# Performance work log

Measured on AMD Instinct MI355X. Metric: run time of the kernel, lower is better.

Reference implementation:

```python
import jax, jax.numpy as jnp
import numpy as np

B, N, D, U, S = 32, 1024, 2, 64, 2


def setup_inputs() -> dict:
    key = jax.random.key(0)
    ks = jax.random.split(key, 8)
    scale = 1.0 / np.sqrt(N)  # keep diffusion outputs in a sane range
    inputs = jax.random.normal(ks[0], (B, N, D), jnp.float32)
    supports = jax.random.normal(ks[1], (B, N, N, S), jnp.float32) * scale
    h_prev = jax.random.normal(ks[2], (B, N * U), jnp.float32)
    rows = (D + U) * (S + 1)  # 198
    wscale = 1.0 / np.sqrt(rows)
    r_kernel = jax.random.normal(ks[3], (rows, U), jnp.float32) * wscale
    u_kernel = jax.random.normal(ks[4], (rows, U), jnp.float32) * wscale
    c_kernel = jax.random.normal(ks[5], (rows, U), jnp.float32) * wscale
    zeros = jnp.zeros((U,), jnp.float32)
    return {"inputs": inputs, "supports": supports, "h_prev": h_prev,
            "r_kernel": r_kernel, "r_bias": zeros,
            "u_kernel": u_kernel, "u_bias": zeros,
            "c_kernel": c_kernel, "c_bias": zeros}


def _diff_conv(x_in, supports, state, kernel, bias):
    # x_in: (B,N,D), state: (B, N*U) -> output (B, N*U)
    b, n, _ = x_in.shape
    u = kernel.shape[1]
    x0 = jnp.concatenate([x_in, state.reshape(b, n, u)], axis=-1)  # (B,N,F)
    # batched graph diffusion for all S supports at once: (B,N,N,S)x(B,N,F)->(B,N,F,S)
    xm = jnp.einsum('bijs,bjf->bifs', supports, x0)
    x = jnp.concatenate([x0[..., None], xm], axis=-1)  # (B,N,F,M) matches tf stack+transpose order
    x = x.reshape(b * n, -1) @ kernel + bias  # (B*N, U)
    return x.reshape(b, n * u)


def reference(inputs, supports, h_prev, r_kernel, r_bias, u_kernel, u_bias, c_kernel, c_bias):
    r = jax.nn.sigmoid(_diff_conv(inputs, supports, h_prev, r_kernel, r_bias))
    u = jax.nn.sigmoid(_diff_conv(inputs, supports, h_prev, u_kernel, u_bias))
    c = jnp.tanh(_diff_conv(inputs, supports, r * h_prev, c_kernel, c_bias))
    h = u * h_prev + (1.0 - u) * c
    return h
```

## Files before the change

### kernel.cpp

```cpp
#include <hip/hip_runtime.h>
#include <hip/hip_bf16.h>

namespace {

constexpr int kN  = 1024;
constexpr int kU  = 64;
constexpr int kFP = 80;

typedef __attribute__((ext_vector_type(4))) float f32x4;
typedef __attribute__((ext_vector_type(8))) short sv8;
typedef unsigned int u32;
typedef unsigned short u16;

__device__ __forceinline__ u32 pack_bf2(float a, float b) {
  __hip_bfloat16 ha = __float2bfloat16(a);
  __hip_bfloat16 hb = __float2bfloat16(b);
  u16 ua = *reinterpret_cast<u16*>(&ha);
  u16 ub = *reinterpret_cast<u16*>(&hb);
  return (u32)ua | ((u32)ub << 16);
}

__device__ __forceinline__ u16 bf16bits(float a) {
  __hip_bfloat16 h = __float2bfloat16(a);
  return *reinterpret_cast<u16*>(&h);
}

__device__ __forceinline__ float bflo(u32 v) {
  u32 x = v << 16;
  return *reinterpret_cast<float*>(&x);
}
__device__ __forceinline__ float bfhi(u32 v) {
  u32 x = v & 0xffff0000u;
  return *reinterpret_cast<float*>(&x);
}

__device__ __forceinline__ void gl16(const void* g, void* l) {
  __builtin_amdgcn_global_load_lds(
      (const __attribute__((address_space(1))) u32*)g,
      (__attribute__((address_space(3))) u32*)l, 16, 0, 0);
}

__global__ __launch_bounds__(256) void convert_sup(
    const f32x4* __restrict__ sup4, uint2* __restrict__ outb) {
  const size_t n4 = (size_t)16 * 1024 * 1024;
  size_t idx = (size_t)blockIdx.x * 256 + threadIdx.x;
  const size_t stride = (size_t)gridDim.x * 256;
#pragma unroll 1
  for (; idx < n4; idx += stride) {
    f32x4 v = __builtin_nontemporal_load(sup4 + idx);
    uint2 o;
    o.x = pack_bf2(v[0], v[1]);
    o.y = pack_bf2(v[2], v[3]);
    outb[idx] = o;
  }
}

__global__ __launch_bounds__(256) void build_x0t(
    const float* __restrict__ inputs, const float* __restrict__ h_prev,
    __hip_bfloat16* __restrict__ x0t, __hip_bfloat16* __restrict__ x0tc) {
  const int bx = blockIdx.x;
  const int b  = bx >> 4;
  const int n0 = (bx & 15) * 64;
  const int t  = threadIdx.x;

  __shared__ float hp[64][65];

  const float* hpg = h_prev + (size_t)b * kN * kU + (size_t)n0 * kU;
#pragma unroll
  for (int r = 0; r < 16; ++r) {
    int idx = t + (r << 8);
    hp[idx >> 6][idx & 63] = hpg[idx];
  }
  __syncthreads();

  {
    int u = t >> 2, g = t & 3;
    __hip_bfloat16* dst = x0t + ((size_t)b * kFP + 2 + u) * kN + n0 + g * 16;
#pragma unroll
    for (int k = 0; k < 16; ++k) dst[k] = __float2bfloat16(hp[g * 16 + k][u]);
  }

  if (t < 128) {
    int d = t & 1, nn = t >> 1;
    float v = inputs[((size_t)b * kN + n0 + nn) * 2 + d];
    __hip_bfloat16 bv = __float2bfloat16(v);
    x0t [((size_t)b * kFP + d) * kN + n0 + nn] = bv;
    x0tc[((size_t)b * kFP + d) * kN + n0 + nn] = bv;
  } else {
    int i2 = t - 128;
    __hip_bfloat16 z = __float2bfloat16(0.0f);
#pragma unroll
    for (int r = 0; r < 7; ++r) {
      int idx = i2 + r * 128;
      int row = 66 + (idx >> 6), nn = idx & 63;
      x0t [((size_t)b * kFP + row) * kN + n0 + nn] = z;
      x0tc[((size_t)b * kFP + row) * kN + n0 + nn] = z;
    }
  }
}

__global__ __launch_bounds__(512, 4) void einsum_diff(
    const u32* __restrict__ supb, const __hip_bfloat16* __restrict__ x0t,
    u16* __restrict__ xfeat) {
  const int bx = blockIdx.x;
  const int wk = (bx & 7) * 64 + (bx >> 3);
  const int b  = wk >> 4;
  const int i0 = (wk & 15) << 6;
  const int t    = threadIdx.x;
  const int lane = t & 63;
  const int w    = t >> 6;
  const int q    = lane >> 4;
  const int lm   = lane & 15;
  const int s    = w & 1;
  const int ih   = w >> 1;

  __shared__ u16 Af[2][2][2][4][64][8];
  __shared__ u16 Xf[2][10][64][8];

  f32x4 acc[5];
#pragma unroll
  for (int n = 0; n < 5; ++n) acc[n] = (f32x4){0.f, 0.f, 0.f, 0.f};

  const u32* sb = supb + ((size_t)b * kN + i0) * kN;
  const u16* xg = reinterpret_cast<const u16*>(x0t) + (size_t)b * kFP * kN;

  const int ii = t >> 3, jb = t & 7;
  const u32* aSrc = sb + (size_t)ii * kN + jb * 8;
  const int ksA = jb >> 2, q2 = jb & 3;
  const int ihhA = ii >> 4, lm2 = ii & 15;
  const int aOff = ksA * 4096 + ihhA * 1024 +
                   (((q2 * 16 + lm2) * 16) ^ (q2 << 4) ^ (ksA << 6));
  char* const afBase = (char*)&Af[0][0][0][0][0][0];

  const int seg1 = w;
  const int seg2 = w + 8;
  const u16* xs1 =
      xg + (size_t)((seg1 % 5) * 16 + lm) * kN + (seg1 / 5) * 32 + q * 8;
  const u16* xs2 = (w < 2)
      ? xg + (size_t)((seg2 % 5) * 16 + lm) * kN + (seg2 / 5) * 32 + q * 8
      : nullptr;

  uint4 W1, W2;

  auto dmaX = [&](int nb, int T) {
    int jo = T * 64;
    gl16(xs1 + jo, &Xf[nb][seg1][0][0]);
    if (w < 2) gl16(xs2 + jo, &Xf[nb][seg2][0][0]);
  };

  auto loadA = [&](int T) {
    const u32* p = aSrc + T * 64;
    W1 = *reinterpret_cast<const uint4*>(p);
    W2 = *reinterpret_cast<const uint4*>(p + 4);
  };

  auto packWrite = [&](int nb) {
    u32 p0[4], p1[4];
    p0[0] = (W1.x & 0xffffu) | (W1.y << 16);
    p0[1] = (W1.z & 0xffffu) | (W1.w << 16);
    p0[2] = (W2.x & 0xffffu) | (W2.y << 16);
    p0[3] = (W2.z & 0xffffu) | (W2.w << 16);
    p1[0] = (W1.x >> 16) | (W1.y & 0xffff0000u);
    p1[1] = (W1.z >> 16) | (W1.w & 0xffff0000u);
    p1[2] = (W2.x >> 16) | (W2.y & 0xffff0000u);
    p1[3] = (W2.z >> 16) | (W2.w & 0xffff0000u);
    char* base = afBase + nb * 16384 + aOff;
    *reinterpret_cast<uint4*>(base)        = (uint4){p0[0], p0[1], p0[2], p0[3]};
    *reinterpret_cast<uint4*>(base + 8192) = (uint4){p1[0], p1[1], p1[2], p1[3]};
  };

  auto compute = [&](int cb_) {
#pragma unroll
    for (int ks = 0; ks < 2; ++ks) {
      const char* ab = afBase + cb_ * 16384 + s * 8192 + ks * 4096 + ih * 1024;
      sv8 a = *reinterpret_cast<const sv8*>(
          ab + (((q * 16 + lm) * 16) ^ (q << 4) ^ (ks << 6)));
#pragma unroll
      for (int n = 0; n < 5; ++n) {
        sv8 xb = *reinterpret_cast<const sv8*>(&Xf[cb_][ks * 5 + n][lane][0]);
        acc[n] = __builtin_amdgcn_mfma_f32_16x16x32_bf16(a, xb, acc[n], 0, 0, 0);
      }
    }
  };

  dmaX(0, 0);
  loadA(0);
  asm volatile("s_waitcnt vmcnt(0)" ::: "memory");
  packWrite(0);
  asm volatile("s_waitcnt lgkmcnt(0)" ::: "memory");
  __builtin_amdgcn_s_barrier();
  __builtin_amdgcn_sched_barrier(0);

#pragma unroll 1
  for (int T = 0; T < 15; ++T) {
    const int nb = (T + 1) & 1;
    dmaX(nb, T + 1);
    loadA(T + 1);
    compute(T & 1);
    asm volatile("s_waitcnt vmcnt(0)" ::: "memory");
    packWrite(nb);
    asm volatile("s_waitcnt lgkmcnt(0)" ::: "memory");
    __builtin_amdgcn_s_barrier();
    __builtin_amdgcn_sched_barrier(0);
  }
  compute(1);
  __syncthreads();

  u16* ep = (u16*)afBase;
#pragma unroll
  for (int n = 0; n < 5; ++n) {
    int f = n * 16 + lm;
    if (f < 66) {
#pragma unroll
      for (int r = 0; r < 4; ++r) {
        int row = ih * 16 + q * 4 + r;
        ep[row * 136 + s * 66 + f] = bf16bits(acc[n][r]);
      }
    }
  }
  __syncthreads();
  const u32* ep32 = reinterpret_cast<const u32*>(ep);
  u32* og = reinterpret_cast<u32*>(xfeat) + ((size_t)b * kN + i0) * 66;
#pragma unroll 1
  for (int g = t; g < 4224; g += 512) {
    int row = g / 66, c = g - row * 66;
    og[g] = ep32[row * 68 + c];
  }
}

__global__ __launch_bounds__(256) void gates_ru(
    const u16* __restrict__ xfeat, const float* __restrict__ rk,
    const float* __restrict__ rbias, const float* __restrict__ uk,
    const float* __restrict__ ubias, const float* __restrict__ inputs,
    const float* __restrict__ h_prev, float* __restrict__ u_buf,
    __hip_bfloat16* __restrict__ x0tc) {
  const int row0 = blockIdx.x * 32;
  const int b = row0 >> 10, n0 = row0 & 1023;
  const int t = threadIdx.x;
  __shared__ float xm[32][134];
  __shared__ float x0s[32][66];

  {
    const u32* xsrc = reinterpret_cast<const u32*>(xfeat) + (size_t)row0 * 66;
#pragma unroll 1
    for (int g = t; g < 2112; g += 256) {
      int row = g / 66, c = g - row * 66;
      u32 v = xsrc[g];
      xm[row][c * 2]     = bflo(v);
      xm[row][c * 2 + 1] = bfhi(v);
    }
  }
#pragma unroll
  for (int r2 = 0; r2 < 8; ++r2) {
    int idx = t + (r2 << 8);
    int rw = idx >> 6, u = idx & 63;
    x0s[rw][2 + u] = h_prev[(size_t)(row0 + rw) * kU + u];
  }
  if (t < 64) x0s[t >> 1][t & 1] = inputs[(size_t)row0 * 2 + t];
  __syncthreads();

  const int cu = t & 15;
  const int rw = (t >> 4) * 2;
  float ar[2][4] = {{0.f,0.f,0.f,0.f},{0.f,0.f,0.f,0.f}};
  float au[2][4] = {{0.f,0.f,0.f,0.f},{0.f,0.f,0.f,0.f}};

#pragma unroll 4
  for (int f = 0; f < 66; ++f) {
    float4 vr = *reinterpret_cast<const float4*>(rk + (size_t)(f * 3) * kU + cu * 4);
    float4 vu = *reinterpret_cast<const float4*>(uk + (size_t)(f * 3) * kU + cu * 4);
    float a0 = x0s[rw][f], a1 = x0s[rw + 1][f];
    ar[0][0] += a0 * vr.x; ar[0][1] += a0 * vr.y; ar[0][2] += a0 * vr.z; ar[0][3] += a0 * vr.w;
    ar[1][0] += a1 * vr.x; ar[1][1] += a1 * vr.y; ar[1][2] += a1 * vr.z; ar[1][3] += a1 * vr.w;
    au[0][0] += a0 * vu.x; au[0][1] += a0 * vu.y; au[0][2] += a0 * vu.z; au[0][3] += a0 * vu.w;
    au[1][0] += a1 * vu.x; au[1][1] += a1 * vu.y; au[1][2] += a1 * vu.z; au[1][3] += a1 * vu.w;
  }
#pragma unroll
  for (int m = 1; m <= 2; ++m) {
#pragma unroll 4
    for (int f = 0; f < 66; ++f) {
      float4 vr = *reinterpret_cast<const float4*>(rk + (size_t)(f * 3 + m) * kU + cu * 4);
      float4 vu = *reinterpret_cast<const float4*>(uk + (size_t)(f * 3 + m) * kU + cu * 4);
      float a0 = xm[rw][(m - 1) * 66 + f], a1 = xm[rw + 1][(m - 1) * 66 + f];
      ar[0][0] += a0 * vr.x; ar[0][1] += a0 * vr.y; ar[0][2] += a0 * vr.z; ar[0][3] += a0 * vr.w;
      ar[1][0] += a1 * vr.x; ar[1][1] += a1 * vr.y; ar[1][2] += a1 * vr.z; ar[1][3] += a1 * vr.w;
      au[0][0] += a0 * vu.x; au[0][1] += a0 * vu.y; au[0][2] += a0 * vu.z; au[0][3] += a0 * vu.w;
      au[1][0] += a1 * vu.x; au[1][1] += a1 * vu.y; au[1][2] += a1 * vu.z; au[1][3] += a1 * vu.w;
    }
  }

#pragma unroll
  for (int rr = 0; rr < 2; ++rr) {
    int grow = row0 + rw + rr;
    int n = n0 + rw + rr;
#pragma unroll
    for (int j = 0; j < 4; ++j) {
      int u = cu * 4 + j;
      float rv = 1.f / (1.f + __expf(-(ar[rr][j] + rbias[u])));
      float uv = 1.f / (1.f + __expf(-(au[rr][j] + ubias[u])));
      u_buf[(size_t)grow * kU + u] = uv;
      float rh = rv * h_prev[(size_t)grow * kU + u];
      x0tc[((size_t)b * kFP + 2 + u) * kN + n] = __float2bfloat16(rh);
    }
  }
}

__global__ __launch_bounds__(256) void gate_c_final(
    const u16* __restrict__ xfeat, const float* __restrict__ ck,
    const float* __restrict__ cbias, const float* __restrict__ inputs,
    const __hip_bfloat16* __restrict__ x0tc, const float* __restrict__ h_prev,
    const float* __restrict__ u_buf, float* __restrict__ out) {
  const int row0 = blockIdx.x * 32;
  const int b = row0 >> 10, n0 = row0 & 1023;
  const int t = threadIdx.x;
  __shared__ float xm[32][134];
  __shared__ float x0c[32][66];

  {
    const u32* xsrc = reinterpret_cast<const u32*>(xfeat) + (size_t)row0 * 66;
#pragma unroll 1
    for (int g = t; g < 2112; g += 256) {
      int row = g / 66, c = g - row * 66;
      u32 v = xsrc[g];
      xm[row][c * 2]     = bflo(v);
      xm[row][c * 2 + 1] = bfhi(v);
    }
  }
#pragma unroll
  for (int r2 = 0; r2 < 8; ++r2) {
    int idx = t + (r2 << 8);
    int u = idx >> 5, nn = idx & 31;
    x0c[nn][2 + u] =
        __bfloat162float(x0tc[((size_t)b * kFP + 2 + u) * kN + n0 + nn]);
  }
  if (t < 64) x0c[t >> 1][t & 1] = inputs[(size_t)row0 * 2 + t];
  __syncthreads();

  const int cu = t & 15;
  const int rw = (t >> 4) * 2;
  float ac[2][4] = {{0.f,0.f,0.f,0.f},{0.f,0.f,0.f,0.f}};

#pragma unroll 4
  for (int f = 0; f < 66; ++f) {
    float4 vc = *reinterpret_cast<const float4*>(ck + (size_t)(f * 3) * kU + cu * 4);
    float a0 = x0c[rw][f], a1 = x0c[rw + 1][f];
    ac[0][0] += a0 * vc.x; ac[0][1] += a0 * vc.y; ac[0][2] += a0 * vc.z; ac[0][3] += a0 * vc.w;
    ac[1][0] += a1 * vc.x; ac[1][1] += a1 * vc.y; ac[1][2] += a1 * vc.z; ac[1][3] += a1 * vc.w;
  }
#pragma unroll
  for (int m = 1; m <= 2; ++m) {
#pragma unroll 4
    for (int f = 0; f < 66; ++f) {
      float4 vc = *reinterpret_cast<const float4*>(ck + (size_t)(f * 3 + m) * kU + cu * 4);
      float a0 = xm[rw][(m - 1) * 66 + f], a1 = xm[rw + 1][(m - 1) * 66 + f];
      ac[0][0] += a0 * vc.x; ac[0][1] += a0 * vc.y; ac[0][2] += a0 * vc.z; ac[0][3] += a0 * vc.w;
      ac[1][0] += a1 * vc.x; ac[1][1] += a1 * vc.y; ac[1][2] += a1 * vc.z; ac[1][3] += a1 * vc.w;
    }
  }

#pragma unroll
  for (int rr = 0; rr < 2; ++rr) {
    int grow = row0 + rw + rr;
#pragma unroll
    for (int j = 0; j < 4; ++j) {
      int u = cu * 4 + j;
      float cv = tanhf(ac[rr][j] + cbias[u]);
      float uv = u_buf[(size_t)grow * kU + u];
      float hp = h_prev[(size_t)grow * kU + u];
      out[(size_t)grow * kU + u] = uv * hp + (1.f - uv) * cv;
    }
  }
}

}

extern "C" void kernel_launch(void* const* d_in, const int* in_sizes, int n_in,
                              void* d_out, int out_size, void* d_ws, size_t ws_size,
                              hipStream_t stream) {
  const float* inputs = (const float*)d_in[0];
  const float* sup    = (const float*)d_in[1];
  const float* h_prev = (const float*)d_in[2];
  const float* rk     = (const float*)d_in[3];
  const float* rbias  = (const float*)d_in[4];
  const float* uk     = (const float*)d_in[5];
  const float* ubias  = (const float*)d_in[6];
  const float* ck     = (const float*)d_in[7];
  const float* cbias  = (const float*)d_in[8];
  float* out = (float*)d_out;

  char* ws = (char*)d_ws;
  __hip_bfloat16* x0t   = (__hip_bfloat16*)(ws);
  __hip_bfloat16* x0tc  = (__hip_bfloat16*)(ws + 5242880);
  u16*            xfeat = (u16*)(ws + 10485760);
  float*          u_buf = (float*)(ws + 19136512);
  u32*            supb  = (u32*)(ws + 27525120);

  hipLaunchKernelGGL(convert_sup, dim3(4096), dim3(256), 0, stream,
                     (const f32x4*)sup, (uint2*)supb);
  hipLaunchKernelGGL(build_x0t, dim3(512), dim3(256), 0, stream,
                     inputs, h_prev, x0t, x0tc);
  hipLaunchKernelGGL(einsum_diff, dim3(512), dim3(512), 0, stream,
                     supb, x0t, xfeat);
  hipLaunchKernelGGL(gates_ru, dim3(1024), dim3(256), 0, stream,
                     xfeat, rk, rbias, uk, ubias, inputs, h_prev, u_buf, x0tc);
  hipLaunchKernelGGL(einsum_diff, dim3(512), dim3(512), 0, stream,
                     supb, x0tc, xfeat);
  hipLaunchKernelGGL(gate_c_final, dim3(1024), dim3(256), 0, stream,
                     xfeat, ck, cbias, inputs, x0tc, h_prev, u_buf, out);
}
```

Before: 223.3 us.

## Triple-buffer LDS tiles with two-deep prefetch and fully unrolled main loop

Changes the A (supports) and X shared-memory staging from double to triple buffering, so global loads run two tiles ahead of the MFMA compute. Partial vmcnt waits let the newest tile's loads stay in flight while the current one is packed. The 16-step loop is fully unrolled through a macro, with each barrier placed after compute. This aims to hide global-load latency better, but raises LDS use per block from about 52KB to about 78KB, which can lower the number of resident blocks per CU. It also adds register pressure from the extra prefetch registers.

```diff
diff --git a/kernel.cpp b/kernel.cpp
--- a/kernel.cpp
+++ b/kernel.cpp
@@ -114,8 +114,8 @@
   const int s    = w & 1;
   const int ih   = w >> 1;
 
-  __shared__ u16 Af[2][2][2][4][64][8];
-  __shared__ u16 Xf[2][10][64][8];
+  __shared__ u16 Af[3][8192];
+  __shared__ u16 Xf[3][10][64][8];
 
   f32x4 acc[5];
 #pragma unroll
@@ -130,7 +130,7 @@
   const int ihhA = ii >> 4, lm2 = ii & 15;
   const int aOff = ksA * 4096 + ihhA * 1024 +
                    (((q2 * 16 + lm2) * 16) ^ (q2 << 4) ^ (ksA << 6));
-  char* const afBase = (char*)&Af[0][0][0][0][0][0];
+  char* const afBase = (char*)&Af[0][0];
 
   const int seg1 = w;
   const int seg2 = w + 8;
@@ -140,71 +140,83 @@
       ? xg + (size_t)((seg2 % 5) * 16 + lm) * kN + (seg2 / 5) * 32 + q * 8
       : nullptr;
 
-  uint4 W1, W2;
-
   auto dmaX = [&](int nb, int T) {
     int jo = T * 64;
     gl16(xs1 + jo, &Xf[nb][seg1][0][0]);
     if (w < 2) gl16(xs2 + jo, &Xf[nb][seg2][0][0]);
   };
 
-  auto loadA = [&](int T) {
+  uint4 WA[3], WB[3];
+
+  auto loadA = [&](uint4& A1, uint4& A2, int T) {
     const u32* p = aSrc + T * 64;
-    W1 = *reinterpret_cast<const uint4*>(p);
-    W2 = *reinterpret_cast<const uint4*>(p + 4);
+    A1 = *reinterpret_cast<const uint4*>(p);
+    A2 = *reinterpret_cast<const uint4*>(p + 4);
   };
 
-  auto packWrite = [&](int nb) {
+  auto packW = [&](const uint4& A1, const uint4& A2, int nb) {
     u32 p0[4], p1[4];
-    p0[0] = (W1.x & 0xffffu) | (W1.y << 16);
-    p0[1] = (W1.z & 0xffffu) | (W1.w << 16);
-    p0[2] = (W2.x & 0xffffu) | (W2.y << 16);
-    p0[3] = (W2.z & 0xffffu) | (W2.w << 16);
-    p1[0] = (W1.x >> 16) | (W1.y & 0xffff0000u);
-    p1[1] = (W1.z >> 16) | (W1.w & 0xffff0000u);
-    p1[2] = (W2.x >> 16) | (W2.y & 0xffff0000u);
-    p1[3] = (W2.z >> 16) | (W2.w & 0xffff0000u);
+    p0[0] = (A1.x & 0xffffu) | (A1.y << 16);
+    p0[1] = (A1.z & 0xffffu) | (A1.w << 16);
+    p0[2] = (A2.x & 0xffffu) | (A2.y << 16);
+    p0[3] = (A2.z & 0xffffu) | (A2.w << 16);
+    p1[0] = (A1.x >> 16) | (A1.y & 0xffff0000u);
+    p1[1] = (A1.z >> 16) | (A1.w & 0xffff0000u);
+    p1[2] = (A2.x >> 16) | (A2.y & 0xffff0000u);
+    p1[3] = (A2.z >> 16) | (A2.w & 0xffff0000u);
     char* base = afBase + nb * 16384 + aOff;
     *reinterpret_cast<uint4*>(base)        = (uint4){p0[0], p0[1], p0[2], p0[3]};
     *reinterpret_cast<uint4*>(base + 8192) = (uint4){p1[0], p1[1], p1[2], p1[3]};
   };
 
-  auto compute = [&](int cb_) {
+  auto compute = [&](int nb) {
 #pragma unroll
     for (int ks = 0; ks < 2; ++ks) {
-      const char* ab = afBase + cb_ * 16384 + s * 8192 + ks * 4096 + ih * 1024;
+      const char* ab = afBase + nb * 16384 + s * 8192 + ks * 4096 + ih * 1024;
       sv8 a = *reinterpret_cast<const sv8*>(
           ab + (((q * 16 + lm) * 16) ^ (q << 4) ^ (ks << 6)));
 #pragma unroll
       for (int n = 0; n < 5; ++n) {
-        sv8 xb = *reinterpret_cast<const sv8*>(&Xf[cb_][ks * 5 + n][lane][0]);
+        sv8 xb = *reinterpret_cast<const sv8*>(&Xf[nb][ks * 5 + n][lane][0]);
         acc[n] = __builtin_amdgcn_mfma_f32_16x16x32_bf16(a, xb, acc[n], 0, 0, 0);
       }
     }
   };
 
-  dmaX(0, 0);
-  loadA(0);
-  asm volatile("s_waitcnt vmcnt(0)" ::: "memory");
-  packWrite(0);
+  dmaX(0, 0); loadA(WA[0], WB[0], 0);
+  dmaX(1, 1); loadA(WA[1], WB[1], 1);
+  if (w < 2) { asm volatile("s_waitcnt vmcnt(4)" ::: "memory"); }
+  else       { asm volatile("s_waitcnt vmcnt(3)" ::: "memory"); }
+  packW(WA[0], WB[0], 0);
   asm volatile("s_waitcnt lgkmcnt(0)" ::: "memory");
   __builtin_amdgcn_s_barrier();
   __builtin_amdgcn_sched_barrier(0);
 
-#pragma unroll 1
-  for (int T = 0; T < 15; ++T) {
-    const int nb = (T + 1) & 1;
-    dmaX(nb, T + 1);
-    loadA(T + 1);
-    compute(T & 1);
-    asm volatile("s_waitcnt vmcnt(0)" ::: "memory");
-    packWrite(nb);
-    asm volatile("s_waitcnt lgkmcnt(0)" ::: "memory");
-    __builtin_amdgcn_s_barrier();
-    __builtin_amdgcn_sched_barrier(0);
-  }
-  compute(1);
-  __syncthreads();
+#define STEP(T)                                                             \
+  {                                                                         \
+    if ((T) + 2 <= 15) {                                                    \
+      dmaX(((T) + 2) % 3, (T) + 2);                                         \
+      loadA(WA[((T) + 2) % 3], WB[((T) + 2) % 3], (T) + 2);                 \
+      if (w < 2) { asm volatile("s_waitcnt vmcnt(4)" ::: "memory"); }       \
+      else       { asm volatile("s_waitcnt vmcnt(3)" ::: "memory"); }       \
+    } else if ((T) + 1 <= 15) {                                             \
+      asm volatile("s_waitcnt vmcnt(0)" ::: "memory");                      \
+    }                                                                       \
+    if ((T) + 1 <= 15) {                                                    \
+      packW(WA[((T) + 1) % 3], WB[((T) + 1) % 3], ((T) + 1) % 3);           \
+      asm volatile("s_waitcnt lgkmcnt(0)" ::: "memory");                    \
+    }                                                                       \
+    __builtin_amdgcn_sched_barrier(0);                                      \
+    compute((T) % 3);                                                       \
+    __builtin_amdgcn_s_barrier();                                           \
+    __builtin_amdgcn_sched_barrier(0);                                      \
+  }
+
+  STEP(0)  STEP(1)  STEP(2)  STEP(3)
+  STEP(4)  STEP(5)  STEP(6)  STEP(7)
+  STEP(8)  STEP(9)  STEP(10) STEP(11)
+  STEP(12) STEP(13) STEP(14) STEP(15)
+#undef STEP
 
   u16* ep = (u16*)afBase;
 #pragma unroll
```

New measurement: 211.3 us, median of 2. 1.06x faster.

## Pre-swizzle bf16 supports into MFMA fragment layout and DMA directly to LDS

Applied to the files above, without the earlier changes.

The conversion kernel now transposes supports through shared memory and writes bf16 in the exact per-tile fragment order the einsum kernel consumes, split by support index. The einsum kernel then loads A tiles with direct global-to-LDS DMA instead of register loads, unpack/pack and LDS stores. Its pipeline is restructured to wait with partial vmcnt and two barriers per step. This removes per-call repacking ALU work and register staging in both einsum launches. In exchange the conversion kernel does more work and synchronisation, and the occupancy hint on the einsum kernel is dropped.

```diff
diff --git a/kernel.cpp b/kernel.cpp
--- a/kernel.cpp
+++ b/kernel.cpp
@@ -41,17 +41,49 @@
 }
 
 __global__ __launch_bounds__(256) void convert_sup(
-    const f32x4* __restrict__ sup4, uint2* __restrict__ outb) {
-  const size_t n4 = (size_t)16 * 1024 * 1024;
-  size_t idx = (size_t)blockIdx.x * 256 + threadIdx.x;
-  const size_t stride = (size_t)gridDim.x * 256;
+    const f32x4* __restrict__ sup4, u16* __restrict__ supb) {
+  const int bx = blockIdx.x;
+  const int b  = bx >> 6;
+  const int rg = bx & 63;
+  const int tile = rg >> 2, w = rg & 3;
+  const int t  = threadIdx.x;
+  const int l64 = t & 63, tg = t >> 6;
+  const int T2 = l64 >> 5, ks = (l64 >> 4) & 1, q = (l64 >> 2) & 3;
+  const int e  = (l64 & 3) * 2;
+
+  __shared__ u16 CL[4096];
+
+  const size_t rowbase = (size_t)(b * 1024 + rg * 16) * 512;
+  u16* const outbase =
+      supb + ((size_t)((b * 16 + tile) * 2)) * 65536 + w * 512;
+
 #pragma unroll 1
-  for (; idx < n4; idx += stride) {
-    f32x4 v = __builtin_nontemporal_load(sup4 + idx);
-    uint2 o;
-    o.x = pack_bf2(v[0], v[1]);
-    o.y = pack_bf2(v[2], v[3]);
-    outb[idx] = o;
+  for (int jc = 0; jc < 8; ++jc) {
+    f32x4 v0 = __builtin_nontemporal_load(sup4 + rowbase + (size_t)(tg) * 512 + jc * 64 + l64);
+    f32x4 v1 = __builtin_nontemporal_load(sup4 + rowbase + (size_t)(tg + 4) * 512 + jc * 64 + l64);
+    f32x4 v2 = __builtin_nontemporal_load(sup4 + rowbase + (size_t)(tg + 8) * 512 + jc * 64 + l64);
+    f32x4 v3 = __builtin_nontemporal_load(sup4 + rowbase + (size_t)(tg + 12) * 512 + jc * 64 + l64);
+    const int ob = T2 * 1024 + ks * 512 + q * 8 + e;
+    *reinterpret_cast<u32*>(&CL[ob + (tg) * 32])           = pack_bf2(v0[0], v0[2]);
+    *reinterpret_cast<u32*>(&CL[2048 + ob + (tg) * 32])    = pack_bf2(v0[1], v0[3]);
+    *reinterpret_cast<u32*>(&CL[ob + (tg + 4) * 32])       = pack_bf2(v1[0], v1[2]);
+    *reinterpret_cast<u32*>(&CL[2048 + ob + (tg + 4) * 32])= pack_bf2(v1[1], v1[3]);
+    *reinterpret_cast<u32*>(&CL[ob + (tg + 8) * 32])       = pack_bf2(v2[0], v2[2]);
+    *reinterpret_cast<u32*>(&CL[2048 + ob + (tg + 8) * 32])= pack_bf2(v2[1], v2[3]);
+    *reinterpret_cast<u32*>(&CL[ob + (tg + 12) * 32])      = pack_bf2(v3[0], v3[2]);
+    *reinterpret_cast<u32*>(&CL[2048 + ob + (tg + 12) * 32])= pack_bf2(v3[1], v3[3]);
+    __syncthreads();
+#pragma unroll
+    for (int pi2 = 0; pi2 < 2; ++pi2) {
+      int pi = tg + pi2 * 4;
+      int so = pi >> 2, T2o = (pi >> 1) & 1, kso = pi & 1;
+      uint4 d = *reinterpret_cast<const uint4*>(
+          &CL[so * 2048 + T2o * 1024 + kso * 512 + (l64 & 15) * 32 + (l64 >> 4) * 8]);
+      u16* dst = outbase + (size_t)so * 65536 + (jc * 2 + T2o) * 4096 +
+                 kso * 2048 + (size_t)l64 * 8;
+      *reinterpret_cast<uint4*>(dst) = d;
+    }
+    __syncthreads();
   }
 }
 
@@ -99,20 +131,21 @@
   }
 }
 
-__global__ __launch_bounds__(512, 4) void einsum_diff(
-    const u32* __restrict__ supb, const __hip_bfloat16* __restrict__ x0t,
+__global__ __launch_bounds__(512) void einsum_diff(
+    const u16* __restrict__ supb, const __hip_bfloat16* __restrict__ x0t,
     u16* __restrict__ xfeat) {
   const int bx = blockIdx.x;
   const int wk = (bx & 7) * 64 + (bx >> 3);
-  const int b  = wk >> 4;
-  const int i0 = (wk & 15) << 6;
+  const int b    = wk >> 4;
+  const int tile = wk & 15;
+  const int i0   = tile * 64;
   const int t    = threadIdx.x;
   const int lane = t & 63;
-  const int w    = t >> 6;
+  const int ww   = t >> 6;
   const int q    = lane >> 4;
   const int lm   = lane & 15;
-  const int s    = w & 1;
-  const int ih   = w >> 1;
+  const int s    = ww & 1;
+  const int ih   = ww >> 1;
 
   __shared__ u16 Af[2][2][2][4][64][8];
   __shared__ u16 Xf[2][10][64][8];
@@ -121,92 +154,58 @@
 #pragma unroll
   for (int n = 0; n < 5; ++n) acc[n] = (f32x4){0.f, 0.f, 0.f, 0.f};
 
-  const u32* sb = supb + ((size_t)b * kN + i0) * kN;
+  const u16* asrc = supb + ((size_t)((b * 16 + tile) * 2 + s)) * 65536 +
+                    ih * 512 + (size_t)lane * 8;
   const u16* xg = reinterpret_cast<const u16*>(x0t) + (size_t)b * kFP * kN;
-
-  const int ii = t >> 3, jb = t & 7;
-  const u32* aSrc = sb + (size_t)ii * kN + jb * 8;
-  const int ksA = jb >> 2, q2 = jb & 3;
-  const int ihhA = ii >> 4, lm2 = ii & 15;
-  const int aOff = ksA * 4096 + ihhA * 1024 +
-                   (((q2 * 16 + lm2) * 16) ^ (q2 << 4) ^ (ksA << 6));
-  char* const afBase = (char*)&Af[0][0][0][0][0][0];
-
-  const int seg1 = w;
-  const int seg2 = w + 8;
+  const int seg1 = ww;
+  const int seg2 = ww + 8;
   const u16* xs1 =
       xg + (size_t)((seg1 % 5) * 16 + lm) * kN + (seg1 / 5) * 32 + q * 8;
-  const u16* xs2 = (w < 2)
+  const u16* xs2 = (ww < 2)
       ? xg + (size_t)((seg2 % 5) * 16 + lm) * kN + (seg2 / 5) * 32 + q * 8
       : nullptr;
 
-  uint4 W1, W2;
-
-  auto dmaX = [&](int nb, int T) {
-    int jo = T * 64;
-    gl16(xs1 + jo, &Xf[nb][seg1][0][0]);
-    if (w < 2) gl16(xs2 + jo, &Xf[nb][seg2][0][0]);
+  auto dma = [&](int nb, int T) {
+    gl16(asrc + T * 4096,        &Af[nb][s][0][ih][0][0]);
+    gl16(asrc + T * 4096 + 2048, &Af[nb][s][1][ih][0][0]);
+    gl16(xs1 + T * 64, &Xf[nb][seg1][0][0]);
+    if (ww < 2) gl16(xs2 + T * 64, &Xf[nb][seg2][0][0]);
   };
 
-  auto loadA = [&](int T) {
-    const u32* p = aSrc + T * 64;
-    W1 = *reinterpret_cast<const uint4*>(p);
-    W2 = *reinterpret_cast<const uint4*>(p + 4);
-  };
-
-  auto packWrite = [&](int nb) {
-    u32 p0[4], p1[4];
-    p0[0] = (W1.x & 0xffffu) | (W1.y << 16);
-    p0[1] = (W1.z & 0xffffu) | (W1.w << 16);
-    p0[2] = (W2.x & 0xffffu) | (W2.y << 16);
-    p0[3] = (W2.z & 0xffffu) | (W2.w << 16);
-    p1[0] = (W1.x >> 16) | (W1.y & 0xffff0000u);
-    p1[1] = (W1.z >> 16) | (W1.w & 0xffff0000u);
-    p1[2] = (W2.x >> 16) | (W2.y & 0xffff0000u);
-    p1[3] = (W2.z >> 16) | (W2.w & 0xffff0000u);
-    char* base = afBase + nb * 16384 + aOff;
-    *reinterpret_cast<uint4*>(base)        = (uint4){p0[0], p0[1], p0[2], p0[3]};
-    *reinterpret_cast<uint4*>(base + 8192) = (uint4){p1[0], p1[1], p1[2], p1[3]};
-  };
-
-  auto compute = [&](int cb_) {
+  auto compute = [&](int nb) {
 #pragma unroll
     for (int ks = 0; ks < 2; ++ks) {
-      const char* ab = afBase + cb_ * 16384 + s * 8192 + ks * 4096 + ih * 1024;
-      sv8 a = *reinterpret_cast<const sv8*>(
-          ab + (((q * 16 + lm) * 16) ^ (q << 4) ^ (ks << 6)));
+      sv8 a = *reinterpret_cast<const sv8*>(&Af[nb][s][ks][ih][lane][0]);
 #pragma unroll
       for (int n = 0; n < 5; ++n) {
-        sv8 xb = *reinterpret_cast<const sv8*>(&Xf[cb_][ks * 5 + n][lane][0]);
+        sv8 xb = *reinterpret_cast<const sv8*>(&Xf[nb][ks * 5 + n][lane][0]);
         acc[n] = __builtin_amdgcn_mfma_f32_16x16x32_bf16(a, xb, acc[n], 0, 0, 0);
       }
     }
   };
 
-  dmaX(0, 0);
-  loadA(0);
+  dma(0, 0);
   asm volatile("s_waitcnt vmcnt(0)" ::: "memory");
-  packWrite(0);
-  asm volatile("s_waitcnt lgkmcnt(0)" ::: "memory");
   __builtin_amdgcn_s_barrier();
   __builtin_amdgcn_sched_barrier(0);
 
 #pragma unroll 1
-  for (int T = 0; T < 15; ++T) {
-    const int nb = (T + 1) & 1;
-    dmaX(nb, T + 1);
-    loadA(T + 1);
-    compute(T & 1);
-    asm volatile("s_waitcnt vmcnt(0)" ::: "memory");
-    packWrite(nb);
-    asm volatile("s_waitcnt lgkmcnt(0)" ::: "memory");
+  for (int T = 0; T < 16; ++T) {
+    if (T + 1 <= 15) {
+      dma((T + 1) & 1, T + 1);
+      if (ww < 2) { asm volatile("s_waitcnt vmcnt(4)" ::: "memory"); }
+      else        { asm volatile("s_waitcnt vmcnt(3)" ::: "memory"); }
+    } else {
+      asm volatile("s_waitcnt vmcnt(0)" ::: "memory");
+    }
     __builtin_amdgcn_s_barrier();
     __builtin_amdgcn_sched_barrier(0);
-  }
-  compute(1);
-  __syncthreads();
-
-  u16* ep = (u16*)afBase;
+    compute(T & 1);
+    __builtin_amdgcn_s_barrier();
+    __builtin_amdgcn_sched_barrier(0);
+  }
+
+  u16* ep = &Af[0][0][0][0][0][0];
 #pragma unroll
   for (int n = 0; n < 5; ++n) {
     int f = n * 16 + lm;
@@ -392,10 +391,10 @@
   __hip_bfloat16* x0tc  = (__hip_bfloat16*)(ws + 5242880);
   u16*            xfeat = (u16*)(ws + 10485760);
   float*          u_buf = (float*)(ws + 19136512);
-  u32*            supb  = (u32*)(ws + 27525120);
-
-  hipLaunchKernelGGL(convert_sup, dim3(4096), dim3(256), 0, stream,
-                     (const f32x4*)sup, (uint2*)supb);
+  u16*            supb  = (u16*)(ws + 27525120);
+
+  hipLaunchKernelGGL(convert_sup, dim3(2048), dim3(256), 0, stream,
+                     (const f32x4*)sup, supb);
   hipLaunchKernelGGL(build_x0t, dim3(512), dim3(256), 0, stream,
                      inputs, h_prev, x0t, x0tc);
   hipLaunchKernelGGL(einsum_diff, dim3(512), dim3(512), 0, stream,
```

After: 215.0 us. 3.7% less time.
